# Kernel tuning notes

Measured on AMD Instinct MI355X. Metric: run time of the kernel, lower is better.

The kernel has to match this reference:

```python
import jax, jax.numpy as jnp
import numpy as np

VOCAB = 50000
EMB = 128
HID = 256
H = HID // 2          # per-direction LSTM hidden
L = 59                # labelset size
B = 512
S = 256
START, STOP, PAD_LBL = 57, 58, 0
NEG = -10000.0


def setup_inputs() -> dict:
    key = jax.random.key(0)
    ks = jax.random.split(key, 12)
    inp = {}
    inp["x"] = jax.random.randint(ks[0], (B, S), 0, VOCAB)
    inp["y"] = jax.random.randint(ks[1], (B, S), 1, START)  # real labels only
    emb = jax.random.normal(ks[2], (VOCAB, EMB), jnp.float32) * 0.02
    inp["embed"] = emb.at[0].set(0.0)  # padding_idx=0

    def lstm_p(k):
        k1, k2, k3, k4 = jax.random.split(k, 4)
        s = 1.0 / np.sqrt(H)
        return (jax.random.uniform(k1, (4 * H, EMB), jnp.float32, -s, s),
                jax.random.uniform(k2, (4 * H, H), jnp.float32, -s, s),
                jax.random.uniform(k3, (4 * H,), jnp.float32, -s, s),
                jax.random.uniform(k4, (4 * H,), jnp.float32, -s, s))

    inp["Wih_f"], inp["Whh_f"], inp["bih_f"], inp["bhh_f"] = lstm_p(ks[3])
    inp["Wih_b"], inp["Whh_b"], inp["bih_b"], inp["bhh_b"] = lstm_p(ks[4])
    s = 1.0 / np.sqrt(HID)
    inp["Wout"] = jax.random.uniform(ks[5], (L, HID), jnp.float32, -s, s)
    inp["bout"] = jax.random.uniform(ks[6], (L,), jnp.float32, -s, s)
    T = jax.random.normal(ks[7], (L, L), jnp.float32)
    T = T.at[START, :].set(NEG)
    T = T.at[:, STOP].set(NEG)
    T = T.at[START, PAD_LBL].set(NEG)
    T = T.at[STOP + 1:, PAD_LBL].set(NEG)  # no-op here (STOP+1==L), kept for fidelity
    inp["trans"] = T
    inp["h0"] = jax.random.normal(ks[8], (2, B, H), jnp.float32)
    inp["c0"] = jax.random.normal(ks[9], (2, B, H), jnp.float32)
    return inp


def _lstm_scan(emb_seq, Wih, Whh, bih, bhh, h0, c0):
    # emb_seq: (S, B, E); PyTorch gate order i, f, g, o
    def step(carry, x_t):
        h, c = carry
        g = x_t @ Wih.T + bih + h @ Whh.T + bhh          # (B, 4H)
        i, f, gg, o = jnp.split(g, 4, axis=-1)
        c = jax.nn.sigmoid(f) * c + jax.nn.sigmoid(i) * jnp.tanh(gg)
        h = jax.nn.sigmoid(o) * jnp.tanh(c)
        return (h, c), h
    _, hs = jax.lax.scan(step, (h0, c0), emb_seq)
    return hs  # (S, B, H)


def reference(x, y, embed, Wih_f, Whh_f, bih_f, bhh_f,
              Wih_b, Whh_b, bih_b, bhh_b, Wout, bout, trans, h0, c0):
    # ---- BiLSTM emissions ----
    emb = embed[x]                                   # (B, S, E)
    emb = jnp.transpose(emb, (1, 0, 2))              # (S, B, E)
    hf = _lstm_scan(emb, Wih_f, Whh_f, bih_f, bhh_f, h0[0], c0[0])
    hb = _lstm_scan(emb[::-1], Wih_b, Whh_b, bih_b, bhh_b, h0[1], c0[1])[::-1]
    out = jnp.concatenate([hf, hb], axis=-1)         # (S, B, HID)
    feats = jnp.einsum('sbh,lh->bsl', out, Wout) + bout   # (B, S, L)

    # ---- CRF forward algorithm (log-sum-exp scan over time) ----
    alpha0 = jnp.full((B, L), NEG, feats.dtype).at[:, START].set(0.0)
    feats_t = jnp.transpose(feats, (1, 0, 2))        # (S, B, L)

    def fstep(alpha, f_t):
        # alpha_new[b, j] = f_t[b, j] + logsumexp_i(alpha[b, i] + trans[j, i])
        a = jax.nn.logsumexp(alpha[:, None, :] + trans[None, :, :], axis=2)
        return f_t + a, None

    alpha, _ = jax.lax.scan(fstep, alpha0, feats_t)
    fwd_score = jax.nn.logsumexp(alpha + trans[STOP][None, :], axis=1)  # (B,)

    # ---- gold path score ----
    yprev = jnp.concatenate([jnp.full((B, 1), START, y.dtype), y[:, :-1]], axis=1)
    emit = jnp.take_along_axis(feats, y[..., None], axis=2)[..., 0]     # (B, S)
    tr = trans[y, yprev]                                                # (B, S)
    gold = emit.sum(axis=1) + tr.sum(axis=1) + trans[STOP, y[:, -1]]

    return jnp.sum(fwd_score - gold)
```

## Files before the change

kernel.cpp:

```cpp
#include <hip/hip_runtime.h>

#define BB   512
#define SS   256
#define EE   128
#define HH   128
#define LL   59
#define STARTL 57
#define STOPL  58
#define VOCAB 50000

typedef float  f32x4  __attribute__((ext_vector_type(4)));
typedef short  bf16x8 __attribute__((ext_vector_type(8)));
typedef short  s16x4  __attribute__((ext_vector_type(4)));

__device__ __forceinline__ short f2bf(float f) {
    unsigned u = __float_as_uint(f);
    u += 0x7FFFu + ((u >> 16) & 1u);
    return (short)(u >> 16);
}
__device__ __forceinline__ float bf2f(unsigned short s) {
    return __uint_as_float(((unsigned)s) << 16);
}
__device__ __forceinline__ float sigf(float x) {
    float e = __builtin_amdgcn_exp2f(-1.44269504f * x);
    return __builtin_amdgcn_rcpf(1.0f + e);
}
__device__ __forceinline__ float tanhf_(float x) {
    float e = __builtin_amdgcn_exp2f(2.88539008f * x);
    return 1.0f - 2.0f * __builtin_amdgcn_rcpf(e + 1.0f);
}
__device__ __forceinline__ float wmax64(float v) {
    #pragma unroll
    for (int o = 32; o; o >>= 1) v = fmaxf(v, __shfl_xor(v, o));
    return v;
}
__device__ __forceinline__ float wsum64(float v) {
    #pragma unroll
    for (int o = 32; o; o >>= 1) v += __shfl_xor(v, o);
    return v;
}
__device__ __forceinline__ float rlane(float v, int i) {
    return __uint_as_float(__builtin_amdgcn_readlane(__float_as_uint(v), i));
}
__device__ __forceinline__ void bar_lds() {
    asm volatile("s_waitcnt lgkmcnt(0)\n\ts_barrier" ::: "memory");
}

__global__ __launch_bounds__(256) void conv_k(
    const float* __restrict__ embed,
    const float* __restrict__ Wih_f, const float* __restrict__ Wih_b,
    const float* __restrict__ Whh_f, const float* __restrict__ Whh_b,
    const float* __restrict__ bih_f, const float* __restrict__ bhh_f,
    const float* __restrict__ bih_b, const float* __restrict__ bhh_b,
    unsigned short* __restrict__ ebf, unsigned short* __restrict__ wix,
    unsigned short* __restrict__ whb, float* __restrict__ bsum)
{
    const int W1 = VOCAB * EE / 4;
    const int W2 = W1 + 2 * 16384;
    const int W3 = W2 + 2 * 16384;
    const int W4 = W3 + 1024;
    for (int i = blockIdx.x * blockDim.x + threadIdx.x; i < W4;
         i += gridDim.x * blockDim.x) {
        if (i < W1) {
            float4 v = ((const float4*)embed)[i];
            s16x4 s = { f2bf(v.x), f2bf(v.y), f2bf(v.z), f2bf(v.w) };
            ((s16x4*)ebf)[i] = s;
        } else if (i < W2) {
            const int j = i - W1, d = j >> 14, e = j & 16383;
            float4 v = ((const float4*)(d ? Wih_b : Wih_f))[e];
            s16x4 s = { f2bf(v.x), f2bf(v.y), f2bf(v.z), f2bf(v.w) };
            ((s16x4*)wix)[d * 16384 + e] = s;
        } else if (i < W3) {
            const int j = i - W2, d = j >> 14, e = j & 16383;
            float4 v = ((const float4*)(d ? Whh_b : Whh_f))[e];
            s16x4 s = { f2bf(v.x), f2bf(v.y), f2bf(v.z), f2bf(v.w) };
            ((s16x4*)whb)[d * 16384 + e] = s;
        } else {
            const int m = i - W3, d = m >> 9, c = m & 511;
            bsum[d * 512 + c] = d ? (bih_b[c] + bhh_b[c]) : (bih_f[c] + bhh_f[c]);
        }
    }
}

__global__ __launch_bounds__(512, 2) void lstm_f(
    const int* __restrict__ x, const unsigned short* __restrict__ ebf,
    const unsigned short* __restrict__ wix, const unsigned short* __restrict__ whb,
    const float* __restrict__ bsum,
    const float* __restrict__ h0, const float* __restrict__ c0,
    const float* __restrict__ Wout,
    unsigned short* __restrict__ fpF, unsigned short* __restrict__ fpB)
{
    const int tid = threadIdx.x;
    const int w = tid >> 6, l = tid & 63, qd = l >> 4, n = l & 15;
    const int rt = blockIdx.x & 127, dir = blockIdx.x >> 7;
    const int b0 = rt * 4;
    unsigned short* fp = dir ? fpB : fpF;

    __shared__ __align__(16) short hbuf[2][2048];
    __shared__ __align__(16) float gxb[2][4][2048];
    __shared__ int xsh[4 * 256];

    #pragma unroll
    for (int i = 0; i < 2; ++i) ((s16x4*)hbuf)[tid + i * 512] = (s16x4)0;
    #pragma unroll
    for (int i = 0; i < 2; ++i) {
        const int k = tid + i * 512;
        xsh[k] = x[(size_t)(b0 + (k >> 8)) * SS + (k & 255)];
    }

    if (w < 4) {
        const int s0 = 2 * w, s1 = 2 * w + 1;
        bf16x8 fh0[4][4], fh1[4][4];
        #pragma unroll
        for (int g = 0; g < 4; ++g) {
            #pragma unroll
            for (int kk = 0; kk < 4; ++kk) {
                fh0[g][kk] = *(const bf16x8*)(whb + dir * 65536
                             + (size_t)(g * 128 + 16 * s0 + n) * 128 + kk * 32 + qd * 8);
                fh1[g][kk] = *(const bf16x8*)(whb + dir * 65536
                             + (size_t)(g * 128 + 16 * s1 + n) * 128 + kk * 32 + qd * 8);
            }
        }
        float cst0 = c0[((size_t)dir * BB + b0 + qd) * HH + 16 * s0 + n];
        float cst1 = c0[((size_t)dir * BB + b0 + qd) * HH + 16 * s1 + n];

        __syncthreads();
        {
            const int j = tid >> 7, c = tid & 127;
            hbuf[0][((c >> 3) * 16 + 4 * j) * 8 + (c & 7)] =
                f2bf(h0[((size_t)dir * BB + b0 + j) * HH + c]);
        }
        __syncthreads();

        const int hid0 = 16 * s0 + n, hc0 = hid0 >> 3, ho0 = hid0 & 7;
        const int hid1 = 16 * s1 + n, hc1 = hid1 >> 3, ho1 = hid1 & 7;
        const int gs0 = (s0 * 64 + qd * 16 + n) * 4;
        const int gs1 = (s1 * 64 + qd * 16 + n) * 4;

        f32x4 a0[4], a1[4];
        #pragma unroll
        for (int g = 0; g < 4; ++g) {
            a0[g] = (f32x4){0.f, 0.f, 0.f, 0.f};
            a1[g] = (f32x4){0.f, 0.f, 0.f, 0.f};
        }

        for (int ts = 0; ts < SS; ++ts) {
            const int cur = ts & 1, nxt = cur ^ 1;
            const int gbuf = (ts >> 2) & 1, tau = ts & 3;

            const f32x4 g0 = *(const f32x4*)&gxb[gbuf][tau][gs0];
            const f32x4 g1 = *(const f32x4*)&gxb[gbuf][tau][gs1];

            bf16x8 ah[4];
            #pragma unroll
            for (int kk = 0; kk < 4; ++kk)
                ah[kk] = *(const bf16x8*)&hbuf[cur][((kk * 4 + qd) * 16 + n) * 8];

            a0[0][0] = g0[0]; a0[1][0] = g0[1]; a0[2][0] = g0[2]; a0[3][0] = g0[3];
            a1[0][0] = g1[0]; a1[1][0] = g1[1]; a1[2][0] = g1[2]; a1[3][0] = g1[3];

            #pragma unroll
            for (int kk = 0; kk < 4; ++kk) {
                #pragma unroll
                for (int g = 0; g < 4; ++g) {
                    a0[g] = __builtin_amdgcn_mfma_f32_16x16x32_bf16(ah[kk], fh0[g][kk], a0[g], 0, 0, 0);
                    a1[g] = __builtin_amdgcn_mfma_f32_16x16x32_bf16(ah[kk], fh1[g][kk], a1[g], 0, 0, 0);
                }
            }

            {
                const float iv0 = sigf(a0[0][0]), fv0 = sigf(a0[1][0]);
                const float gv0 = tanhf_(a0[2][0]), ov0 = sigf(a0[3][0]);
                const float cc0 = fv0 * cst0 + iv0 * gv0;
                cst0 = cc0;
                hbuf[nxt][(hc0 * 16 + 4 * qd) * 8 + ho0] = f2bf(ov0 * tanhf_(cc0));
                const float iv1 = sigf(a1[0][0]), fv1 = sigf(a1[1][0]);
                const float gv1 = tanhf_(a1[2][0]), ov1 = sigf(a1[3][0]);
                const float cc1 = fv1 * cst1 + iv1 * gv1;
                cst1 = cc1;
                hbuf[nxt][(hc1 * 16 + 4 * qd) * 8 + ho1] = f2bf(ov1 * tanhf_(cc1));
            }
            bar_lds();
        }
    } else {
        const int ct = w - 4;
        const int s0 = 2 * (w - 4), s1 = s0 + 1;
        bf16x8 fx0[4][4], fx1[4][4]; float bs0[4], bs1[4];
        #pragma unroll
        for (int g = 0; g < 4; ++g) {
            bs0[g] = bsum[dir * 512 + g * 128 + 16 * s0 + n];
            bs1[g] = bsum[dir * 512 + g * 128 + 16 * s1 + n];
            #pragma unroll
            for (int kk = 0; kk < 4; ++kk) {
                fx0[g][kk] = *(const bf16x8*)(wix + dir * 65536
                             + (size_t)(g * 128 + 16 * s0 + n) * 128 + kk * 32 + qd * 8);
                fx1[g][kk] = *(const bf16x8*)(wix + dir * 65536
                             + (size_t)(g * 128 + 16 * s1 + n) * 128 + kk * 32 + qd * 8);
            }
        }
        bf16x8 wbx[4];
        {
            const int col = ct * 16 + n;
            #pragma unroll
            for (int kk = 0; kk < 4; ++kk) {
                bf16x8 v = (bf16x8)0;
                if (col < LL) {
                    const float* p = Wout + (size_t)col * 256 + dir * 128 + kk * 32 + qd * 8;
                    #pragma unroll
                    for (int j = 0; j < 8; ++j) v[j] = f2bf(p[j]);
                }
                wbx[kk] = v;
            }
        }
        const int gs0 = (s0 * 64 + qd * 16 + n) * 4;
        const int gs1 = (s1 * 64 + qd * 16 + n) * 4;
        const int jb   = n >> 2;
        const int tau  = n & 3;
        const int jrow = jb * 256;

        unsigned short* fpx = fp + ((size_t)(b0 + qd) * SS + (dir ? SS - 1 : 0)) * 64
                            + ct * 16 + n;
        const ptrdiff_t fpd = dir ? -64 : 64;

        auto loadfrag = [&](int G, bf16x8* e) {
            const int t  = 4 * G + tau;
            const int te = dir ? (SS - 1 - t) : t;
            const int xi = xsh[jrow + te];
            const unsigned short* er = ebf + (size_t)xi * EE + qd * 8;
            e[0] = *(const bf16x8*)(er);
            e[1] = *(const bf16x8*)(er + 32);
            e[2] = *(const bf16x8*)(er + 64);
            e[3] = *(const bf16x8*)(er + 96);
        };
        auto computeS = [&](const bf16x8* e, const bf16x8 (*fx)[4],
                            const float* bs, int gsv, int buf) {
            f32x4 c[4] = { {0,0,0,0}, {0,0,0,0}, {0,0,0,0}, {0,0,0,0} };
            #pragma unroll
            for (int g = 0; g < 4; ++g) {
                #pragma unroll
                for (int kk = 0; kk < 4; ++kk)
                    c[g] = __builtin_amdgcn_mfma_f32_16x16x32_bf16(e[kk], fx[g][kk], c[g], 0, 0, 0);
            }
            #pragma unroll
            for (int r = 0; r < 4; ++r) {
                f32x4 p = { c[0][r] + bs[0], c[1][r] + bs[1],
                            c[2][r] + bs[2], c[3][r] + bs[3] };
                *(f32x4*)&gxb[buf][r][gsv] = p;
            }
        };
        auto projx = [&](int ts) {
            f32x4 pp = (f32x4){0.f, 0.f, 0.f, 0.f};
            #pragma unroll
            for (int kk = 0; kk < 4; ++kk) {
                const bf16x8 a = *(const bf16x8*)&hbuf[ts & 1][((kk * 4 + qd) * 16 + n) * 8];
                pp = __builtin_amdgcn_mfma_f32_16x16x32_bf16(a, wbx[kk], pp, 0, 0, 0);
            }
            *fpx = (unsigned short)f2bf(pp[0]);
            fpx += fpd;
        };

        __syncthreads();
        bf16x8 eA[4], eB[4];
        loadfrag(0, eA);
        computeS(eA, fx0, bs0, gs0, 0);
        computeS(eA, fx1, bs1, gs1, 0);
        loadfrag(1, eB);
        __syncthreads();

        auto xgroup = [&](int G, bf16x8* use, bf16x8* pre) {
            const int t0 = 4 * G;
            if (G + 2 < SS / 4) loadfrag(G + 2, pre);
            if (G + 1 < SS / 4) computeS(use, fx0, bs0, gs0, (G + 1) & 1);
            if (t0 > 0) projx(t0);
            bar_lds();
            if (G + 1 < SS / 4) computeS(use, fx1, bs1, gs1, (G + 1) & 1);
            projx(t0 + 1);
            bar_lds();
            projx(t0 + 2);
            bar_lds();
            projx(t0 + 3);
            bar_lds();
        };
        for (int G = 0; G < SS / 4; G += 2) {
            xgroup(G,     eB, eA);
            xgroup(G + 1, eA, eB);
        }
        projx(SS);
    }
}

__global__ __launch_bounds__(128, 1) void crf_k(
    const unsigned short* __restrict__ fpF, const unsigned short* __restrict__ fpB,
    const float* __restrict__ bout, const int* __restrict__ y,
    const float* __restrict__ trans, float* __restrict__ out)
{
    const int tid = threadIdx.x;
    const int wv = tid >> 6;
    const int j = tid & 63;
    const int b = blockIdx.x;
    const size_t bS = (size_t)b * SS;
    const bool valid = (j < LL);
    const int  jr = valid ? j : (LL - 1);
    const float L2E = 1.44269504f, LN2 = 0.69314718f;

    __shared__ float exch[64];
    __shared__ float gshare;

    float etr[LL];
    #pragma unroll
    for (int i = 0; i < LL; ++i) {
        const float t = wv ? trans[i * LL + jr] : trans[jr * LL + i];
        etr[i] = valid ? __builtin_amdgcn_exp2f(t * L2E) : 0.0f;
    }
    const float bo = valid ? bout[jr] : 0.0f;

    float st;
    if (wv == 0) st = valid ? ((j == STARTL) ? 0.0f : -10000.0f * L2E) : -1e30f;
    else         st = valid ? trans[STOPL * LL + jr] * L2E : -1e30f;
    float Kn = 0.0f;

    auto tAt = [&](int u) { return wv ? (SS - 1 - u) : u; };

    float fF[8], fB[8];
    #pragma unroll
    for (int q = 0; q < 8; ++q) {
        const int t = tAt(q);
        fF[q] = bf2f(fpF[(bS + t) * 64 + j]);
        fB[q] = bf2f(fpB[(bS + t) * 64 + j]);
    }

    for (int u0 = 0; u0 < SS / 2; u0 += 8) {
        float nF[8], nB[8];
        #pragma unroll
        for (int q = 0; q < 8; ++q) { nF[q] = 0.0f; nB[q] = 0.0f; }
        if (u0 + 8 < SS / 2) {
            #pragma unroll
            for (int q = 0; q < 8; ++q) {
                const int t = tAt(u0 + 8 + q);
                nF[q] = bf2f(fpF[(bS + t) * 64 + j]);
                nB[q] = bf2f(fpB[(bS + t) * 64 + j]);
            }
        }
        float fs[8];
        #pragma unroll
        for (int q = 0; q < 8; ++q) fs[q] = (fF[q] + fB[q] + bo) * L2E;

        #pragma unroll
        for (int u = 0; u < 8; ++u) {
            if (wv == 0) {
                const float Kc = Kn;
                const float ea = __builtin_amdgcn_exp2f(st - Kc);
                Kn = fmaxf(rlane(st, 1), rlane(st, STARTL));
                float d0 = 0.f, d1 = 0.f, d2 = 0.f, d3 = 0.f;
                float d4 = 0.f, d5 = 0.f, d6 = 0.f, d7 = 0.f;
                #pragma unroll
                for (int i = 0; i < 56; i += 8) {
                    d0 += etr[i]     * rlane(ea, i);
                    d1 += etr[i + 1] * rlane(ea, i + 1);
                    d2 += etr[i + 2] * rlane(ea, i + 2);
                    d3 += etr[i + 3] * rlane(ea, i + 3);
                    d4 += etr[i + 4] * rlane(ea, i + 4);
                    d5 += etr[i + 5] * rlane(ea, i + 5);
                    d6 += etr[i + 6] * rlane(ea, i + 6);
                    d7 += etr[i + 7] * rlane(ea, i + 7);
                }
                d0 += etr[56] * rlane(ea, 56);
                d1 += etr[57] * rlane(ea, 57);
                d2 += etr[58] * rlane(ea, 58);
                const float dot = ((d0 + d1) + (d2 + d3)) + ((d4 + d5) + (d6 + d7));
                st = fs[u] + Kc + __builtin_amdgcn_logf(dot);
            } else {
                const float g = fs[u] + st;
                const float Kc = Kn;
                const float eg = __builtin_amdgcn_exp2f(g - Kc);
                Kn = rlane(g, 1);
                float d0 = 0.f, d1 = 0.f, d2 = 0.f, d3 = 0.f;
                float d4 = 0.f, d5 = 0.f, d6 = 0.f, d7 = 0.f;
                #pragma unroll
                for (int i = 0; i < 56; i += 8) {
                    d0 += etr[i]     * rlane(eg, i);
                    d1 += etr[i + 1] * rlane(eg, i + 1);
                    d2 += etr[i + 2] * rlane(eg, i + 2);
                    d3 += etr[i + 3] * rlane(eg, i + 3);
                    d4 += etr[i + 4] * rlane(eg, i + 4);
                    d5 += etr[i + 5] * rlane(eg, i + 5);
                    d6 += etr[i + 6] * rlane(eg, i + 6);
                    d7 += etr[i + 7] * rlane(eg, i + 7);
                }
                d0 += etr[56] * rlane(eg, 56);
                d1 += etr[57] * rlane(eg, 57);
                d2 += etr[58] * rlane(eg, 58);
                const float dot = ((d0 + d1) + (d2 + d3)) + ((d4 + d5) + (d6 + d7));
                st = Kc + __builtin_amdgcn_logf(dot);
            }
        }
        #pragma unroll
        for (int q = 0; q < 8; ++q) { fF[q] = nF[q]; fB[q] = nB[q]; }
    }

    if (wv == 1) {
        float g = 0.0f;
        #pragma unroll
        for (int q = 0; q < 4; ++q) {
            const int t  = q * 64 + j;
            const int yt = y[bS + t];
            const int yp = t ? y[bS + t - 1] : STARTL;
            g += bf2f(fpF[(bS + t) * 64 + yt]) + bf2f(fpB[(bS + t) * 64 + yt])
               + bout[yt] + trans[yt * LL + yp];
        }
        g = wsum64(g);
        if (j == 0) {
            g += trans[STOPL * LL + y[bS + SS - 1]];
            gshare = g;
        }
        exch[j] = st;
    }
    __syncthreads();
    if (wv == 0) {
        const float v2 = valid ? (st + exch[j]) : -1e30f;
        const float m2 = wmax64(v2);
        const float s  = wsum64(__builtin_amdgcn_exp2f(v2 - m2));
        const float fwd = LN2 * (m2 + __builtin_amdgcn_logf(s));
        if (j == 0) atomicAdd(out, fwd - gshare);
    }
}

extern "C" void kernel_launch(void* const* d_in, const int* in_sizes, int n_in,
                              void* d_out, int out_size, void* d_ws, size_t ws_size,
                              hipStream_t stream)
{
    (void)in_sizes; (void)n_in; (void)out_size; (void)ws_size;
    const int*   x      = (const int*)  d_in[0];
    const int*   y      = (const int*)  d_in[1];
    const float* embed  = (const float*)d_in[2];
    const float* Wih_f  = (const float*)d_in[3];
    const float* Whh_f  = (const float*)d_in[4];
    const float* bih_f  = (const float*)d_in[5];
    const float* bhh_f  = (const float*)d_in[6];
    const float* Wih_b  = (const float*)d_in[7];
    const float* Whh_b  = (const float*)d_in[8];
    const float* bih_b  = (const float*)d_in[9];
    const float* bhh_b  = (const float*)d_in[10];
    const float* Wout   = (const float*)d_in[11];
    const float* bout   = (const float*)d_in[12];
    const float* trans  = (const float*)d_in[13];
    const float* h0     = (const float*)d_in[14];
    const float* c0     = (const float*)d_in[15];

    const size_t MiB = 1ull << 20;
    unsigned short* fpF  = (unsigned short*)d_ws;
    unsigned short* fpB  = (unsigned short*)((char*)d_ws + 16 * MiB);
    unsigned short* ebf  = (unsigned short*)((char*)d_ws + 32 * MiB);
    unsigned short* wix  = (unsigned short*)((char*)d_ws + 45 * MiB);
    unsigned short* whb  = (unsigned short*)((char*)d_ws + 45 * MiB + 256 * 1024);
    float*          bsum = (float*)((char*)d_ws + 45 * MiB + 512 * 1024);

    hipMemsetAsync(d_out, 0, sizeof(float), stream);
    conv_k<<<2048, 256, 0, stream>>>(embed, Wih_f, Wih_b, Whh_f, Whh_b,
                                     bih_f, bhh_f, bih_b, bhh_b,
                                     ebf, wix, whb, bsum);
    lstm_f<<<256, 512, 0, stream>>>(x, ebf, wix, whb, bsum, h0, c0, Wout,
                                    fpF, fpB);
    crf_k<<<BB, 128, 0, stream>>>(fpF, fpB, bout, y, trans, (float*)d_out);
}
```

Baseline: 332.7 us.

## Ring-buffer LSTM hidden state and spread output projection across four steps

The LSTM hidden-state LDS buffer grows from 2 to 8 slots, so the helper waves can project four timesteps of h at once with a single batched MFMA chain. That chain is split across the four per-step barriers, and the input-gate GEMM is also split into halves per barrier to even out helper work between syncs. The recurrent waves now run the MFMAs and gate math for the first hidden slice before starting the second, so activation math can overlap the remaining matrix work. The cost is more LDS for hbuf, which may lower occupancy, plus more intricate indexing that has to stay consistent with the ring slots.

```diff
diff --git a/kernel.cpp b/kernel.cpp
--- a/kernel.cpp
+++ b/kernel.cpp
@@ -96,12 +96,12 @@
     const int b0 = rt * 4;
     unsigned short* fp = dir ? fpB : fpF;
 
-    __shared__ __align__(16) short hbuf[2][2048];
+    __shared__ __align__(16) short hbuf[8][2048];
     __shared__ __align__(16) float gxb[2][4][2048];
     __shared__ int xsh[4 * 256];
 
     #pragma unroll
-    for (int i = 0; i < 2; ++i) ((s16x4*)hbuf)[tid + i * 512] = (s16x4)0;
+    for (int i = 0; i < 8; ++i) ((s16x4*)hbuf)[tid + i * 512] = (s16x4)0;
     #pragma unroll
     for (int i = 0; i < 2; ++i) {
         const int k = tid + i * 512;
@@ -145,7 +145,7 @@
         }
 
         for (int ts = 0; ts < SS; ++ts) {
-            const int cur = ts & 1, nxt = cur ^ 1;
+            const int cur = ts & 7, nxt = (ts + 1) & 7;
             const int gbuf = (ts >> 2) & 1, tau = ts & 3;
 
             const f32x4 g0 = *(const f32x4*)&gxb[gbuf][tau][gs0];
@@ -162,18 +162,23 @@
             #pragma unroll
             for (int kk = 0; kk < 4; ++kk) {
                 #pragma unroll
-                for (int g = 0; g < 4; ++g) {
+                for (int g = 0; g < 4; ++g)
                     a0[g] = __builtin_amdgcn_mfma_f32_16x16x32_bf16(ah[kk], fh0[g][kk], a0[g], 0, 0, 0);
-                    a1[g] = __builtin_amdgcn_mfma_f32_16x16x32_bf16(ah[kk], fh1[g][kk], a1[g], 0, 0, 0);
-                }
-            }
-
+            }
             {
                 const float iv0 = sigf(a0[0][0]), fv0 = sigf(a0[1][0]);
                 const float gv0 = tanhf_(a0[2][0]), ov0 = sigf(a0[3][0]);
                 const float cc0 = fv0 * cst0 + iv0 * gv0;
                 cst0 = cc0;
                 hbuf[nxt][(hc0 * 16 + 4 * qd) * 8 + ho0] = f2bf(ov0 * tanhf_(cc0));
+            }
+            #pragma unroll
+            for (int kk = 0; kk < 4; ++kk) {
+                #pragma unroll
+                for (int g = 0; g < 4; ++g)
+                    a1[g] = __builtin_amdgcn_mfma_f32_16x16x32_bf16(ah[kk], fh1[g][kk], a1[g], 0, 0, 0);
+            }
+            {
                 const float iv1 = sigf(a1[0][0]), fv1 = sigf(a1[1][0]);
                 const float gv1 = tanhf_(a1[2][0]), ov1 = sigf(a1[3][0]);
                 const float cc1 = fv1 * cst1 + iv1 * gv1;
@@ -217,10 +222,7 @@
         const int jb   = n >> 2;
         const int tau  = n & 3;
         const int jrow = jb * 256;
-
-        unsigned short* fpx = fp + ((size_t)(b0 + qd) * SS + (dir ? SS - 1 : 0)) * 64
-                            + ct * 16 + n;
-        const ptrdiff_t fpd = dir ? -64 : 64;
+        const short* hflat = &hbuf[0][0];
 
         auto loadfrag = [&](int G, bf16x8* e) {
             const int t  = 4 * G + tau;
@@ -232,15 +234,7 @@
             e[2] = *(const bf16x8*)(er + 64);
             e[3] = *(const bf16x8*)(er + 96);
         };
-        auto computeS = [&](const bf16x8* e, const bf16x8 (*fx)[4],
-                            const float* bs, int gsv, int buf) {
-            f32x4 c[4] = { {0,0,0,0}, {0,0,0,0}, {0,0,0,0}, {0,0,0,0} };
-            #pragma unroll
-            for (int g = 0; g < 4; ++g) {
-                #pragma unroll
-                for (int kk = 0; kk < 4; ++kk)
-                    c[g] = __builtin_amdgcn_mfma_f32_16x16x32_bf16(e[kk], fx[g][kk], c[g], 0, 0, 0);
-            }
+        auto gxStore = [&](const f32x4* c, const float* bs, int gsv, int buf) {
             #pragma unroll
             for (int r = 0; r < 4; ++r) {
                 f32x4 p = { c[0][r] + bs[0], c[1][r] + bs[1],
@@ -248,44 +242,121 @@
                 *(f32x4*)&gxb[buf][r][gsv] = p;
             }
         };
-        auto projx = [&](int ts) {
-            f32x4 pp = (f32x4){0.f, 0.f, 0.f, 0.f};
-            #pragma unroll
-            for (int kk = 0; kk < 4; ++kk) {
-                const bf16x8 a = *(const bf16x8*)&hbuf[ts & 1][((kk * 4 + qd) * 16 + n) * 8];
-                pp = __builtin_amdgcn_mfma_f32_16x16x32_bf16(a, wbx[kk], pp, 0, 0, 0);
-            }
-            *fpx = (unsigned short)f2bf(pp[0]);
-            fpx += fpd;
+        auto projStore = [&](const f32x4& pp, int P) {
+            const int t0 = 4 * P;
+            #pragma unroll
+            for (int r = 0; r < 4; ++r) {
+                const int t = t0 + r;
+                const int tep = dir ? (SS - 1 - t) : t;
+                fp[((size_t)(b0 + qd) * SS + tep) * 64 + ct * 16 + n]
+                    = (unsigned short)f2bf(pp[r]);
+            }
         };
 
         __syncthreads();
         bf16x8 eA[4], eB[4];
         loadfrag(0, eA);
-        computeS(eA, fx0, bs0, gs0, 0);
-        computeS(eA, fx1, bs1, gs1, 0);
+        {
+            f32x4 c[4] = { {0,0,0,0}, {0,0,0,0}, {0,0,0,0}, {0,0,0,0} };
+            #pragma unroll
+            for (int g = 0; g < 4; ++g)
+                #pragma unroll
+                for (int kk = 0; kk < 4; ++kk)
+                    c[g] = __builtin_amdgcn_mfma_f32_16x16x32_bf16(eA[kk], fx0[g][kk], c[g], 0, 0, 0);
+            gxStore(c, bs0, gs0, 0);
+            #pragma unroll
+            for (int g = 0; g < 4; ++g) c[g] = (f32x4){0.f, 0.f, 0.f, 0.f};
+            #pragma unroll
+            for (int g = 0; g < 4; ++g)
+                #pragma unroll
+                for (int kk = 0; kk < 4; ++kk)
+                    c[g] = __builtin_amdgcn_mfma_f32_16x16x32_bf16(eA[kk], fx1[g][kk], c[g], 0, 0, 0);
+            gxStore(c, bs1, gs1, 0);
+        }
         loadfrag(1, eB);
         __syncthreads();
 
-        auto xgroup = [&](int G, bf16x8* use, bf16x8* pre) {
-            const int t0 = 4 * G;
+        f32x4 c[4], pp;
+        for (int G = 0; G < SS / 4; ++G) {
+            const bool prod = (G + 1 < SS / 4);
+            const bool dopj = (G > 0);
+            const int  nb   = (G + 1) & 1;
+            const int  P    = G - 1;
+            const int pbase = (int)(((unsigned)(4 * P + tau + 1) & 7u) * 2048u)
+                            + qd * 128 + 32 * jb;
+            bf16x8* use = (G & 1) ? eA : eB;
+            bf16x8* pre = (G & 1) ? eB : eA;
+
             if (G + 2 < SS / 4) loadfrag(G + 2, pre);
-            if (G + 1 < SS / 4) computeS(use, fx0, bs0, gs0, (G + 1) & 1);
-            if (t0 > 0) projx(t0);
+            if (prod) {
+                #pragma unroll
+                for (int g = 0; g < 4; ++g) c[g] = (f32x4){0.f, 0.f, 0.f, 0.f};
+                #pragma unroll
+                for (int kk = 0; kk < 2; ++kk)
+                    #pragma unroll
+                    for (int g = 0; g < 4; ++g)
+                        c[g] = __builtin_amdgcn_mfma_f32_16x16x32_bf16(use[kk], fx0[g][kk], c[g], 0, 0, 0);
+            }
+            if (dopj) {
+                pp = (f32x4){0.f, 0.f, 0.f, 0.f};
+                const bf16x8 a = *(const bf16x8*)(hflat + pbase);
+                pp = __builtin_amdgcn_mfma_f32_16x16x32_bf16(a, wbx[0], pp, 0, 0, 0);
+            }
             bar_lds();
-            if (G + 1 < SS / 4) computeS(use, fx1, bs1, gs1, (G + 1) & 1);
-            projx(t0 + 1);
+            if (prod) {
+                #pragma unroll
+                for (int kk = 2; kk < 4; ++kk)
+                    #pragma unroll
+                    for (int g = 0; g < 4; ++g)
+                        c[g] = __builtin_amdgcn_mfma_f32_16x16x32_bf16(use[kk], fx0[g][kk], c[g], 0, 0, 0);
+                gxStore(c, bs0, gs0, nb);
+            }
+            if (dopj) {
+                const bf16x8 a = *(const bf16x8*)(hflat + pbase + 512);
+                pp = __builtin_amdgcn_mfma_f32_16x16x32_bf16(a, wbx[1], pp, 0, 0, 0);
+            }
             bar_lds();
-            projx(t0 + 2);
+            if (prod) {
+                #pragma unroll
+                for (int g = 0; g < 4; ++g) c[g] = (f32x4){0.f, 0.f, 0.f, 0.f};
+                #pragma unroll
+                for (int kk = 0; kk < 2; ++kk)
+                    #pragma unroll
+                    for (int g = 0; g < 4; ++g)
+                        c[g] = __builtin_amdgcn_mfma_f32_16x16x32_bf16(use[kk], fx1[g][kk], c[g], 0, 0, 0);
+            }
+            if (dopj) {
+                const bf16x8 a = *(const bf16x8*)(hflat + pbase + 1024);
+                pp = __builtin_amdgcn_mfma_f32_16x16x32_bf16(a, wbx[2], pp, 0, 0, 0);
+            }
             bar_lds();
-            projx(t0 + 3);
+            if (prod) {
+                #pragma unroll
+                for (int kk = 2; kk < 4; ++kk)
+                    #pragma unroll
+                    for (int g = 0; g < 4; ++g)
+                        c[g] = __builtin_amdgcn_mfma_f32_16x16x32_bf16(use[kk], fx1[g][kk], c[g], 0, 0, 0);
+                gxStore(c, bs1, gs1, nb);
+            }
+            if (dopj) {
+                const bf16x8 a = *(const bf16x8*)(hflat + pbase + 1536);
+                pp = __builtin_amdgcn_mfma_f32_16x16x32_bf16(a, wbx[3], pp, 0, 0, 0);
+                projStore(pp, P);
+            }
             bar_lds();
-        };
-        for (int G = 0; G < SS / 4; G += 2) {
-            xgroup(G,     eB, eA);
-            xgroup(G + 1, eA, eB);
-        }
-        projx(SS);
+        }
+        {
+            const int P = SS / 4 - 1;
+            const int pbase = (int)(((unsigned)(4 * P + tau + 1) & 7u) * 2048u)
+                            + qd * 128 + 32 * jb;
+            pp = (f32x4){0.f, 0.f, 0.f, 0.f};
+            #pragma unroll
+            for (int kk = 0; kk < 4; ++kk) {
+                const bf16x8 a = *(const bf16x8*)(hflat + pbase + kk * 512);
+                pp = __builtin_amdgcn_mfma_f32_16x16x32_bf16(a, wbx[kk], pp, 0, 0, 0);
+            }
+            projStore(pp, P);
+        }
     }
 }
 
```

Result: slower. 350.0 us (+5.2%).
